# Kernel tuning notes

Measured on AMD Instinct MI355X. Metric: run time of the kernel, lower is better.

The kernel has to match this reference:

```python
import jax, jax.numpy as jnp
import numpy as np

N_HEAD = 16
DROP_P = 0.1


def setup_inputs() -> dict:
    key = jax.random.key(0)
    ks = jax.random.split(key, 5)
    B, T, C = 2, 2048, 1024
    return {
        "x": jax.random.normal(ks[0], (B, T, C), dtype=jnp.float32),
        "w_attn": jax.random.normal(ks[1], (C, 3 * C), dtype=jnp.float32) * 0.02,
        "b_attn": jax.random.normal(ks[2], (3 * C,), dtype=jnp.float32) * 0.02,
        "w_proj": jax.random.normal(ks[3], (C, C), dtype=jnp.float32) * 0.02,
        "b_proj": jax.random.normal(ks[4], (C,), dtype=jnp.float32) * 0.02,
    }


def reference(x, w_attn, b_attn, w_proj, b_proj):
    B, T, C = x.shape
    H = N_HEAD
    D = C // H  # head dim
    qkv = x @ w_attn + b_attn                      # [B,T,3C]
    q, k, v = jnp.split(qkv, 3, axis=-1)
    # [B,T,C] -> [B,H,T,D]
    q = q.reshape(B, T, H, D).transpose(0, 2, 1, 3)
    k = k.reshape(B, T, H, D).transpose(0, 2, 1, 3)
    v = v.reshape(B, T, H, D).transpose(0, 2, 1, 3)
    scale = 1.0 / jnp.sqrt(jnp.float32(D))
    attn = jnp.einsum("bhqd,bhkd->bhqk", q, k) * scale  # [B,H,T,T]
    causal = jnp.tril(jnp.ones((T, T), dtype=bool))
    attn = jnp.where(causal[None, None], attn, jnp.float32(-jnp.inf))
    attn = jax.nn.softmax(attn, axis=-1)
    # dropout p=0.1 (training mode in original); deterministic fixed key here
    keep = jax.random.bernoulli(jax.random.key(42), 1.0 - DROP_P, attn.shape)
    attn = jnp.where(keep, attn / (1.0 - DROP_P), 0.0)
    out = jnp.einsum("bhqk,bhkd->bhqd", attn, v)   # [B,H,T,D]
    out = out.transpose(0, 2, 1, 3).reshape(B, T, C)
    return out @ w_proj + b_proj
```

## Files before the change

kernel.cpp:

```cpp
#include <hip/hip_runtime.h>
#include <hip/hip_bf16.h>
#include <stdint.h>
#include <math.h>

#define TSEQ   2048
#define NBATCH 2
#define NHEAD  16
#define HDIM   64
#define CDIM   1024

#define KEEP_THRESH 7549747u

typedef short  bf16x8 __attribute__((ext_vector_type(8)));
typedef float  f32x4  __attribute__((ext_vector_type(4)));

__device__ __forceinline__ uint32_t rotl32(uint32_t x, int r) {
    return __builtin_amdgcn_alignbit(x, x, 32 - r);
}

__device__ __forceinline__ uint32_t tf2x32_xor(uint32_t x0, uint32_t x1) {
    const uint32_t ka = 0u, kb = 42u;
    const uint32_t kc = ka ^ kb ^ 0x1BD11BDAu;
    x0 += ka; x1 += kb;
#define TFR(r) { x0 += x1; x1 = rotl32(x1, r); x1 ^= x0; }
    TFR(13) TFR(15) TFR(26) TFR(6)
    x0 += kb; x1 += kc + 1u;
    TFR(17) TFR(29) TFR(16) TFR(24)
    x0 += kc; x1 += ka + 2u;
    TFR(13) TFR(15) TFR(26) TFR(6)
    x0 += ka; x1 += kb + 3u;
    TFR(17) TFR(29) TFR(16) TFR(24)
    x0 += kb; x1 += kc + 4u;
    TFR(13) TFR(15) TFR(26) TFR(6)
    x0 += kc; x1 += ka + 5u;
#undef TFR
    return x0 ^ x1;
}

__device__ __forceinline__ bool tf_keep(uint32_t idx) {
    return (tf2x32_xor(0u, idx) >> 9) < KEEP_THRESH;
}

__device__ __forceinline__ ushort f2bf(float f) {
    __hip_bfloat16 h = __float2bfloat16(f);
    return *reinterpret_cast<ushort*>(&h);
}

__device__ __forceinline__ void async_copy16(void* lds, const void* g) {
    __builtin_amdgcn_global_load_lds(
        (const __attribute__((address_space(1))) unsigned int*)g,
        (__attribute__((address_space(3))) unsigned int*)lds, 16, 0, 0);
}

__global__ __launch_bounds__(256) void cvt_bf16(
    const float* __restrict__ src, ushort* __restrict__ dst, int n)
{
    int idx = (blockIdx.x * 256 + threadIdx.x) * 8;
    if (idx >= n) return;
    float4 a = *(const float4*)(src + idx);
    float4 b = *(const float4*)(src + idx + 4);
    ushort4 o1; o1.x = f2bf(a.x); o1.y = f2bf(a.y); o1.z = f2bf(a.z); o1.w = f2bf(a.w);
    ushort4 o2; o2.x = f2bf(b.x); o2.y = f2bf(b.y); o2.z = f2bf(b.z); o2.w = f2bf(b.w);
    *(ushort4*)(dst + idx) = o1;
    *(ushort4*)(dst + idx + 4) = o2;
}

__global__ __launch_bounds__(256) void transpose_cvt(
    const float* __restrict__ src, ushort* __restrict__ dst, int K, int N)
{
    __shared__ float t[32][33];
    const int n0 = blockIdx.x * 32, k0 = blockIdx.y * 32;
    const int i = threadIdx.x;
    {
        int k = i >> 3, n4 = (i & 7) * 4;
        float4 v = *(const float4*)(src + (size_t)(k0 + k) * N + n0 + n4);
        t[k][n4 + 0] = v.x; t[k][n4 + 1] = v.y; t[k][n4 + 2] = v.z; t[k][n4 + 3] = v.w;
    }
    __syncthreads();
    {
        int n = i >> 3, k4 = (i & 7) * 4;
        ushort4 o;
        o.x = f2bf(t[k4 + 0][n]); o.y = f2bf(t[k4 + 1][n]);
        o.z = f2bf(t[k4 + 2][n]); o.w = f2bf(t[k4 + 3][n]);
        *(ushort4*)(dst + (size_t)(n0 + n) * K + k0 + k4) = o;
    }
}

template<int MODE>
__global__ __launch_bounds__(256) void gemm_bf16(
    const ushort* __restrict__ A, const ushort* __restrict__ Bt,
    const float* __restrict__ bias,
    ushort* __restrict__ Q, ushort* __restrict__ Kq, ushort* __restrict__ V,
    float* __restrict__ Cf, int M, int N, int K)
{
    __shared__ ushort As[2][128 * 32];
    __shared__ ushort Bs[2][128 * 32];
    const int tid = threadIdx.x, lane = tid & 63, wid = tid >> 6;
    const int l15 = lane & 15, l4 = lane >> 4;
    const int wr = wid >> 1, wc = wid & 1;
    const int bn = blockIdx.x, bm = blockIdx.y;
    const int NTK = K >> 5;

    f32x4 acc[4][4];
#pragma unroll
    for (int m = 0; m < 4; ++m)
#pragma unroll
        for (int n = 0; n < 4; ++n) acc[m][n] = (f32x4){0.f, 0.f, 0.f, 0.f};

    auto stage = [&](int p, int k0) {
#pragma unroll
        for (int j = 0; j < 2; ++j) {
            const int rbase = wid * 32 + j * 16;
            const int row = rbase + (lane >> 2);
            const ushort* src = A + (size_t)(bm * 128 + row) * K + k0 + (lane & 3) * 8;
            async_copy16(&As[p][rbase * 32], src);
        }
#pragma unroll
        for (int j = 0; j < 2; ++j) {
            const int rbase = wid * 32 + j * 16;
            const int row = rbase + (lane >> 2);
            const ushort* src = Bt + (size_t)(bn * 128 + row) * K + k0 + (lane & 3) * 8;
            async_copy16(&Bs[p][rbase * 32], src);
        }
    };
    auto compute = [&](int p) {
        bf16x8 af[4], bf[4];
#pragma unroll
        for (int m = 0; m < 4; ++m)
            af[m] = *(const bf16x8*)&As[p][(wr * 64 + m * 16 + l15) * 32 + l4 * 8];
#pragma unroll
        for (int n = 0; n < 4; ++n)
            bf[n] = *(const bf16x8*)&Bs[p][(wc * 64 + n * 16 + l15) * 32 + l4 * 8];
#pragma unroll
        for (int m = 0; m < 4; ++m)
#pragma unroll
            for (int n = 0; n < 4; ++n)
                acc[m][n] = __builtin_amdgcn_mfma_f32_16x16x32_bf16(af[m], bf[n], acc[m][n], 0, 0, 0);
    };

    stage(0, 0);
    __syncthreads();
    for (int t = 0; t < NTK; ++t) {
        const int p = t & 1;
        if (t + 1 < NTK) stage(p ^ 1, (t + 1) << 5);
        compute(p);
        __syncthreads();
    }

    const int colbase = bn * 128 + wc * 64;
    const int rowbase = bm * 128 + wr * 64;
    if (MODE == 0) {
#pragma unroll
        for (int n = 0; n < 4; ++n) {
            const int col = colbase + n * 16 + l15;
            const float bv = bias[col];
#pragma unroll
            for (int m = 0; m < 4; ++m)
#pragma unroll
                for (int r = 0; r < 4; ++r) {
                    const int row = rowbase + m * 16 + l4 * 4 + r;
                    Cf[(size_t)row * N + col] = acc[m][n][r] + bv;
                }
        }
    } else {
#pragma unroll
        for (int n = 0; n < 4; ++n) {
            const int col = colbase + n * 16 + l15;
            const int which = col >> 10, cc = col & 1023;
            const int hh = cc >> 6, dd = cc & 63;
            const float bv = bias[col];
#pragma unroll
            for (int m = 0; m < 4; ++m)
#pragma unroll
                for (int r = 0; r < 4; ++r) {
                    const int row = rowbase + m * 16 + l4 * 4 + r;
                    const int bb = row >> 11, tt = row & 2047;
                    const ushort val = f2bf(acc[m][n][r] + bv);
                    if (which == 0)
                        Q[(((size_t)(bb * NHEAD + hh)) * TSEQ + tt) * HDIM + dd] = val;
                    else if (which == 1)
                        Kq[(((size_t)(bb * NHEAD + hh)) * TSEQ + tt) * HDIM + dd] = val;
                    else
                        V[(((size_t)(bb * NHEAD + hh)) * HDIM + dd) * TSEQ + tt] = val;
                }
        }
    }
}

__global__ __launch_bounds__(256) void attn_fwd_mfma(
    const ushort* __restrict__ Qb, const ushort* __restrict__ Kb,
    const ushort* __restrict__ VbT, ushort* __restrict__ AO)
{
    __shared__ ushort Ks[2][64 * 64];
    __shared__ ushort Vt[2][64 * 64];
    __shared__ ushort Ps[64 * 64];
    const int tid = threadIdx.x;
    const int lane = tid & 63;
    const int wid = tid >> 6;
    const int l15 = lane & 15, l4 = lane >> 4;
    const int h = blockIdx.y, b = blockIdx.z;
    const int hb = b * NHEAD + h;
    const size_t headoff = (size_t)hb * TSEQ * HDIM;
    const ushort* Qg = Qb + headoff;
    const ushort* Kg = Kb + headoff;
    const ushort* Vg = VbT + headoff;

    auto stage = [&](int p, int kt) {
        const ushort* Kt = Kg + (size_t)(kt * 64) * HDIM;
        const ushort* Vt0 = Vg + kt * 64;
#pragma unroll
        for (int c = 0; c < 2; ++c) {
            const int rbase = wid * 16 + c * 8;
            const int row = rbase + (lane >> 3);
            const ushort* srcK = Kt + row * 64 + (((lane & 7) * 8) ^ ((row & 7) << 3));
            async_copy16(&Ks[p][rbase * 64], srcK);
            const ushort* srcV = Vt0 + (size_t)row * TSEQ + (((lane & 7) * 8) ^ ((row & 7) << 3));
            async_copy16(&Vt[p][rbase * 64], srcV);
        }
    };

    const int swq = (l15 & 7) << 3;
    const int prow = wid * 16 + l15;

    for (int pass = 0; pass < 2; ++pass) {
        const int qt = pass ? (TSEQ / 64 - 1) - (int)blockIdx.x : (int)blockIdx.x;
        const int q0 = qt * 64;
        const int qglob = q0 + wid * 16 + l15;

        bf16x8 qf0, qf1;
        {
            const ushort* qrow = Qg + (size_t)qglob * HDIM;
            qf0 = *(const bf16x8*)(qrow + l4 * 8);
            qf1 = *(const bf16x8*)(qrow + 32 + l4 * 8);
        }

        f32x4 oacc[4];
#pragma unroll
        for (int i = 0; i < 4; ++i) oacc[i] = (f32x4){0.f, 0.f, 0.f, 0.f};
        float mi = -INFINITY, li = 0.f;
        const uint32_t rowbase = ((uint32_t)hb * TSEQ + (uint32_t)qglob) * TSEQ;

        stage(0, 0);
        __syncthreads();

        for (int kt = 0; kt <= qt; ++kt) {
            const int p = kt & 1;
            if (kt < qt) stage(p ^ 1, kt + 1);

            f32x4 s4[4];
#pragma unroll
            for (int ct = 0; ct < 4; ++ct) {
                const int krow = ct * 16 + l15;
                const int sw = (krow & 7) << 3;
                bf16x8 kf0 = *(const bf16x8*)&Ks[p][krow * 64 + ((l4 * 8) ^ sw)];
                bf16x8 kf1 = *(const bf16x8*)&Ks[p][krow * 64 + ((l4 * 8 + 32) ^ sw)];
                f32x4 a = {0.f, 0.f, 0.f, 0.f};
                a = __builtin_amdgcn_mfma_f32_16x16x32_bf16(kf0, qf0, a, 0, 0, 0);
                a = __builtin_amdgcn_mfma_f32_16x16x32_bf16(kf1, qf1, a, 0, 0, 0);
                s4[ct] = a;
            }

            const int kb0 = kt * 64;
            float ev[4][4];
            float mx = -INFINITY;
#pragma unroll
            for (int ct = 0; ct < 4; ++ct)
#pragma unroll
                for (int r = 0; r < 4; ++r) {
                    const int kglob = kb0 + ct * 16 + l4 * 4 + r;
                    const float xx = s4[ct][r] * 0.125f;
                    ev[ct][r] = (kglob <= qglob) ? xx : -INFINITY;
                    mx = fmaxf(mx, ev[ct][r]);
                }
            mx = fmaxf(mx, __shfl_xor(mx, 16));
            mx = fmaxf(mx, __shfl_xor(mx, 32));
            const float mnew = fmaxf(mi, mx);
            const float alpha = __expf(mi - mnew);
            mi = mnew;
            float rs = 0.f;
#pragma unroll
            for (int ct = 0; ct < 4; ++ct)
#pragma unroll
                for (int r = 0; r < 4; ++r) {
                    ev[ct][r] = __expf(ev[ct][r] - mnew);
                    rs += ev[ct][r];
                }
            rs += __shfl_xor(rs, 16);
            rs += __shfl_xor(rs, 32);
            li = li * alpha + rs;
#pragma unroll
            for (int dt = 0; dt < 4; ++dt) {
                oacc[dt][0] *= alpha; oacc[dt][1] *= alpha;
                oacc[dt][2] *= alpha; oacc[dt][3] *= alpha;
            }

            const uint32_t idx0 = rowbase + (uint32_t)kb0;
#pragma unroll
            for (int ct = 0; ct < 4; ++ct) {
                const uint32_t kk = idx0 + (uint32_t)(ct * 16 + l4 * 4);
                ushort4 pk;
                pk.x = f2bf(tf_keep(kk + 0u) ? ev[ct][0] : 0.f);
                pk.y = f2bf(tf_keep(kk + 1u) ? ev[ct][1] : 0.f);
                pk.z = f2bf(tf_keep(kk + 2u) ? ev[ct][2] : 0.f);
                pk.w = f2bf(tf_keep(kk + 3u) ? ev[ct][3] : 0.f);
                *(ushort4*)&Ps[prow * 64 + ((ct * 16 + l4 * 4) ^ swq)] = pk;
            }

            bf16x8 pf0 = *(const bf16x8*)&Ps[prow * 64 + ((l4 * 8) ^ swq)];
            bf16x8 pf1 = *(const bf16x8*)&Ps[prow * 64 + ((l4 * 8 + 32) ^ swq)];
#pragma unroll
            for (int dt = 0; dt < 4; ++dt) {
                const int drow = dt * 16 + l15;
                const int swv = (drow & 7) << 3;
                bf16x8 vf0 = *(const bf16x8*)&Vt[p][drow * 64 + ((l4 * 8) ^ swv)];
                bf16x8 vf1 = *(const bf16x8*)&Vt[p][drow * 64 + ((l4 * 8 + 32) ^ swv)];
                oacc[dt] = __builtin_amdgcn_mfma_f32_16x16x32_bf16(vf0, pf0, oacc[dt], 0, 0, 0);
                oacc[dt] = __builtin_amdgcn_mfma_f32_16x16x32_bf16(vf1, pf1, oacc[dt], 0, 0, 0);
            }
            __syncthreads();
        }

        const float inv = 1.0f / (li * 0.9f);
        ushort* orow = AO + ((size_t)(b * TSEQ + qglob)) * CDIM + h * HDIM;
#pragma unroll
        for (int dt = 0; dt < 4; ++dt) {
            ushort4 o;
            o.x = f2bf(oacc[dt][0] * inv);
            o.y = f2bf(oacc[dt][1] * inv);
            o.z = f2bf(oacc[dt][2] * inv);
            o.w = f2bf(oacc[dt][3] * inv);
            *(ushort4*)&orow[dt * 16 + l4 * 4] = o;
        }
        __syncthreads();
    }
}

extern "C" void kernel_launch(void* const* d_in, const int* in_sizes, int n_in,
                              void* d_out, int out_size, void* d_ws, size_t ws_size,
                              hipStream_t stream)
{
    const float* x      = (const float*)d_in[0];
    const float* w_attn = (const float*)d_in[1];
    const float* b_attn = (const float*)d_in[2];
    const float* w_proj = (const float*)d_in[3];
    const float* b_proj = (const float*)d_in[4];
    float* out = (float*)d_out;

    const size_t NH = (size_t)NBATCH * NHEAD * TSEQ * HDIM;
    ushort* Qb  = (ushort*)d_ws;
    ushort* Kb  = Qb + NH;
    ushort* VbT = Kb + NH;
    ushort* AO  = VbT + NH;
    ushort* xb  = AO + NH;
    ushort* wTa = xb + NH;
    ushort* wTp = wTa + (size_t)3072 * 1024;

    cvt_bf16<<<2048, 256, 0, stream>>>(x, xb, 4096 * 1024);
    transpose_cvt<<<dim3(96, 32), 256, 0, stream>>>(w_attn, wTa, 1024, 3072);
    transpose_cvt<<<dim3(32, 32), 256, 0, stream>>>(w_proj, wTp, 1024, 1024);

    gemm_bf16<1><<<dim3(24, 32), 256, 0, stream>>>(
        xb, wTa, b_attn, Qb, Kb, VbT, nullptr, 4096, 3072, 1024);

    attn_fwd_mfma<<<dim3(TSEQ / 128, NHEAD, NBATCH), 256, 0, stream>>>(Qb, Kb, VbT, AO);

    gemm_bf16<0><<<dim3(8, 32), 256, 0, stream>>>(
        AO, wTp, b_proj, nullptr, nullptr, nullptr, out, 4096, 1024, 1024);
}
```

Measured before the change: 249.7 us.

## Split attention KV range across two blocks with merge kernel and exp2 prescale

Attention work for each query tile is split into two halves of the key range, so the grid doubles from 16 to 32 blocks along x. Each block writes unnormalized partial outputs plus row max and sum into scratch, reusing the output buffer for the partials. A new merge kernel combines the two halves. Q is prescaled by scale*log2(e) in the QKV GEMM so softmax can use exp2f, and the causal mask is applied only on the diagonal tile. This adds an extra kernel launch, extra global traffic for the partials, and bf16 rounding of the partial outputs.

```diff
diff --git a/kernel.cpp b/kernel.cpp
--- a/kernel.cpp
+++ b/kernel.cpp
@@ -10,6 +10,7 @@
 #define CDIM   1024
 
 #define KEEP_THRESH 7549747u
+#define QSC 0.18033688011112042f
 
 typedef short  bf16x8 __attribute__((ext_vector_type(8)));
 typedef float  f32x4  __attribute__((ext_vector_type(4)));
@@ -46,6 +47,10 @@
     return *reinterpret_cast<ushort*>(&h);
 }
 
+__device__ __forceinline__ float bf2f(ushort u) {
+    union { uint32_t i; float f; } c; c.i = ((uint32_t)u) << 16; return c.f;
+}
+
 __device__ __forceinline__ void async_copy16(void* lds, const void* g) {
     __builtin_amdgcn_global_load_lds(
         (const __attribute__((address_space(1))) unsigned int*)g,
@@ -169,13 +174,14 @@
             const int which = col >> 10, cc = col & 1023;
             const int hh = cc >> 6, dd = cc & 63;
             const float bv = bias[col];
+            const float sc = (which == 0) ? QSC : 1.0f;
 #pragma unroll
             for (int m = 0; m < 4; ++m)
 #pragma unroll
                 for (int r = 0; r < 4; ++r) {
                     const int row = rowbase + m * 16 + l4 * 4 + r;
                     const int bb = row >> 11, tt = row & 2047;
-                    const ushort val = f2bf(acc[m][n][r] + bv);
+                    const ushort val = f2bf((acc[m][n][r] + bv) * sc);
                     if (which == 0)
                         Q[(((size_t)(bb * NHEAD + hh)) * TSEQ + tt) * HDIM + dd] = val;
                     else if (which == 1)
@@ -189,7 +195,8 @@
 
 __global__ __launch_bounds__(256) void attn_fwd_mfma(
     const ushort* __restrict__ Qb, const ushort* __restrict__ Kb,
-    const ushort* __restrict__ VbT, ushort* __restrict__ AO)
+    const ushort* __restrict__ VbT,
+    ushort* __restrict__ Ap, float* __restrict__ mp, float* __restrict__ lp)
 {
     __shared__ ushort Ks[2][64 * 64];
     __shared__ ushort Vt[2][64 * 64];
@@ -198,6 +205,7 @@
     const int lane = tid & 63;
     const int wid = tid >> 6;
     const int l15 = lane & 15, l4 = lane >> 4;
+    const int pair = blockIdx.x >> 1, half = blockIdx.x & 1;
     const int h = blockIdx.y, b = blockIdx.z;
     const int hb = b * NHEAD + h;
     const size_t headoff = (size_t)hb * TSEQ * HDIM;
@@ -223,10 +231,25 @@
     const int prow = wid * 16 + l15;
 
     for (int pass = 0; pass < 2; ++pass) {
-        const int qt = pass ? (TSEQ / 64 - 1) - (int)blockIdx.x : (int)blockIdx.x;
-        const int q0 = qt * 64;
-        const int qglob = q0 + wid * 16 + l15;
-
+        const int qt = pass ? (TSEQ / 64 - 1) - pair : pair;
+        const int ntk = qt + 1;
+        const int kb = half ? (ntk + 1) >> 1 : 0;
+        const int ke = half ? ntk : (ntk + 1) >> 1;
+        const int pidx = (hb * 32 + qt) * 2 + half;
+        const int tilerow = wid * 16 + l15;
+        ushort* arow = Ap + (size_t)pidx * 4096 + tilerow * 64;
+
+        if (kb >= ke) {
+#pragma unroll
+            for (int dt = 0; dt < 4; ++dt) {
+                ushort4 z; z.x = z.y = z.z = z.w = 0;
+                *(ushort4*)&arow[dt * 16 + l4 * 4] = z;
+            }
+            if (l4 == 0) { mp[pidx * 64 + tilerow] = -INFINITY; lp[pidx * 64 + tilerow] = 0.f; }
+            continue;
+        }
+
+        const int qglob = qt * 64 + tilerow;
         bf16x8 qf0, qf1;
         {
             const ushort* qrow = Qg + (size_t)qglob * HDIM;
@@ -240,12 +263,12 @@
         float mi = -INFINITY, li = 0.f;
         const uint32_t rowbase = ((uint32_t)hb * TSEQ + (uint32_t)qglob) * TSEQ;
 
-        stage(0, 0);
+        stage(0, kb);
         __syncthreads();
 
-        for (int kt = 0; kt <= qt; ++kt) {
-            const int p = kt & 1;
-            if (kt < qt) stage(p ^ 1, kt + 1);
+        for (int kt = kb; kt < ke; ++kt) {
+            const int p = (kt - kb) & 1;
+            if (kt + 1 < ke) stage(p ^ 1, kt + 1);
 
             f32x4 s4[4];
 #pragma unroll
@@ -263,26 +286,35 @@
             const int kb0 = kt * 64;
             float ev[4][4];
             float mx = -INFINITY;
-#pragma unroll
-            for (int ct = 0; ct < 4; ++ct)
-#pragma unroll
-                for (int r = 0; r < 4; ++r) {
-                    const int kglob = kb0 + ct * 16 + l4 * 4 + r;
-                    const float xx = s4[ct][r] * 0.125f;
-                    ev[ct][r] = (kglob <= qglob) ? xx : -INFINITY;
-                    mx = fmaxf(mx, ev[ct][r]);
-                }
+            if (kt == qt) {
+#pragma unroll
+                for (int ct = 0; ct < 4; ++ct)
+#pragma unroll
+                    for (int r = 0; r < 4; ++r) {
+                        const int kglob = kb0 + ct * 16 + l4 * 4 + r;
+                        ev[ct][r] = (kglob <= qglob) ? s4[ct][r] : -INFINITY;
+                        mx = fmaxf(mx, ev[ct][r]);
+                    }
+            } else {
+#pragma unroll
+                for (int ct = 0; ct < 4; ++ct)
+#pragma unroll
+                    for (int r = 0; r < 4; ++r) {
+                        ev[ct][r] = s4[ct][r];
+                        mx = fmaxf(mx, ev[ct][r]);
+                    }
+            }
             mx = fmaxf(mx, __shfl_xor(mx, 16));
             mx = fmaxf(mx, __shfl_xor(mx, 32));
             const float mnew = fmaxf(mi, mx);
-            const float alpha = __expf(mi - mnew);
+            const float alpha = exp2f(mi - mnew);
             mi = mnew;
             float rs = 0.f;
 #pragma unroll
             for (int ct = 0; ct < 4; ++ct)
 #pragma unroll
                 for (int r = 0; r < 4; ++r) {
-                    ev[ct][r] = __expf(ev[ct][r] - mnew);
+                    ev[ct][r] = exp2f(ev[ct][r] - mnew);
                     rs += ev[ct][r];
                 }
             rs += __shfl_xor(rs, 16);
@@ -320,19 +352,44 @@
             __syncthreads();
         }
 
-        const float inv = 1.0f / (li * 0.9f);
-        ushort* orow = AO + ((size_t)(b * TSEQ + qglob)) * CDIM + h * HDIM;
 #pragma unroll
         for (int dt = 0; dt < 4; ++dt) {
             ushort4 o;
-            o.x = f2bf(oacc[dt][0] * inv);
-            o.y = f2bf(oacc[dt][1] * inv);
-            o.z = f2bf(oacc[dt][2] * inv);
-            o.w = f2bf(oacc[dt][3] * inv);
-            *(ushort4*)&orow[dt * 16 + l4 * 4] = o;
-        }
-        __syncthreads();
+            o.x = f2bf(oacc[dt][0]); o.y = f2bf(oacc[dt][1]);
+            o.z = f2bf(oacc[dt][2]); o.w = f2bf(oacc[dt][3]);
+            *(ushort4*)&arow[dt * 16 + l4 * 4] = o;
+        }
+        if (l4 == 0) { mp[pidx * 64 + tilerow] = mi; lp[pidx * 64 + tilerow] = li; }
     }
+}
+
+__global__ __launch_bounds__(256) void attn_merge(
+    const ushort* __restrict__ Ap, const float* __restrict__ mp,
+    const float* __restrict__ lp, ushort* __restrict__ AO)
+{
+    const int gidx = blockIdx.x * 16 + (threadIdx.x >> 4);
+    const int hb = gidx >> 11;
+    const int q  = gidx & 2047;
+    const int qt = q >> 6, row = q & 63;
+    const int sub = (threadIdx.x & 15) * 4;
+    const int pidx0 = (hb * 32 + qt) * 2;
+    const int pr = pidx0 * 64 + row;
+    const float m0 = mp[pr], m1 = mp[pr + 64];
+    const float l0 = lp[pr], l1 = lp[pr + 64];
+    const float m  = fmaxf(m0, m1);
+    const float w0 = exp2f(m0 - m), w1 = exp2f(m1 - m);
+    const float inv = 1.0f / ((l0 * w0 + l1 * w1) * 0.9f);
+    const float s0 = w0 * inv, s1 = w1 * inv;
+    ushort4 a0 = *(const ushort4*)&Ap[(size_t)pidx0 * 4096 + row * 64 + sub];
+    ushort4 a1 = *(const ushort4*)&Ap[(size_t)(pidx0 + 1) * 4096 + row * 64 + sub];
+    const int b = hb >> 4, h = hb & 15;
+    ushort* orow = AO + ((size_t)(b * TSEQ + q)) * CDIM + h * HDIM + sub;
+    ushort4 o;
+    o.x = f2bf(bf2f(a0.x) * s0 + bf2f(a1.x) * s1);
+    o.y = f2bf(bf2f(a0.y) * s0 + bf2f(a1.y) * s1);
+    o.z = f2bf(bf2f(a0.z) * s0 + bf2f(a1.z) * s1);
+    o.w = f2bf(bf2f(a0.w) * s0 + bf2f(a1.w) * s1);
+    *(ushort4*)orow = o;
 }
 
 extern "C" void kernel_launch(void* const* d_in, const int* in_sizes, int n_in,
@@ -354,6 +411,10 @@
     ushort* xb  = AO + NH;
     ushort* wTa = xb + NH;
     ushort* wTp = wTa + (size_t)3072 * 1024;
+    float*  mp  = (float*)(wTp + (size_t)1024 * 1024);
+    float*  lp  = mp + (size_t)2048 * 64;
+
+    ushort* Aparts = (ushort*)d_out;
 
     cvt_bf16<<<2048, 256, 0, stream>>>(x, xb, 4096 * 1024);
     transpose_cvt<<<dim3(96, 32), 256, 0, stream>>>(w_attn, wTa, 1024, 3072);
@@ -362,7 +423,10 @@
     gemm_bf16<1><<<dim3(24, 32), 256, 0, stream>>>(
         xb, wTa, b_attn, Qb, Kb, VbT, nullptr, 4096, 3072, 1024);
 
-    attn_fwd_mfma<<<dim3(TSEQ / 128, NHEAD, NBATCH), 256, 0, stream>>>(Qb, Kb, VbT, AO);
+    attn_fwd_mfma<<<dim3(32, NHEAD, NBATCH), 256, 0, stream>>>(
+        Qb, Kb, VbT, Aparts, mp, lp);
+
+    attn_merge<<<4096, 256, 0, stream>>>(Aparts, mp, lp, AO);
 
     gemm_bf16<0><<<dim3(8, 32), 256, 0, stream>>>(
         AO, wTp, b_proj, nullptr, nullptr, nullptr, out, 4096, 1024, 1024);
```

Result: no change. 247.1 us (-1.0%).
